# Kernel tuning notes

Measured on AMD Instinct MI355X. Metric: run time of the kernel, lower is better.

Reference implementation:

```python
import jax, jax.numpy as jnp
import numpy as np

B, T, S, D = 8, 16, 256, 1024
H, KVH, HD = 16, 4, 64
GROUPS = H // KVH
SCALE = HD ** -0.5
CAP = 50.0
EPS = 1e-6


def setup_inputs() -> dict:
    key = jax.random.key(0)
    ks = jax.random.split(key, 5)
    return {
        "x": jax.random.normal(ks[0], (B, T, S, D), dtype=jnp.float32),
        "Wq": jax.random.normal(ks[1], (D, H * HD), dtype=jnp.float32) * (D ** -0.5),
        "Wk": jax.random.normal(ks[2], (D, KVH * HD), dtype=jnp.float32) * (D ** -0.5),
        "Wv": jax.random.normal(ks[3], (D, KVH * HD), dtype=jnp.float32) * (D ** -0.5),
        "Wo": jax.random.normal(ks[4], (H * HD, D), dtype=jnp.float32) * ((H * HD) ** -0.5),
        "q_norm_w": jnp.ones((HD,), dtype=jnp.float32),
        "k_norm_w": jnp.ones((HD,), dtype=jnp.float32),
    }


def _rmsnorm(x, w):
    rms = jnp.sqrt(jnp.mean(x * x, axis=-1, keepdims=True) + EPS)
    return x / rms * w


def reference(x, Wq, Wk, Wv, Wo, q_norm_w, k_norm_w):
    b, t, s, d = x.shape
    xf = x.reshape(b * t, s, d)                    # (BT, S, D)
    q = (xf @ Wq).reshape(b * t, s, H, HD).transpose(0, 2, 1, 3)   # (BT, H, S, hd)
    k = (xf @ Wk).reshape(b * t, s, KVH, HD).transpose(0, 2, 1, 3)  # (BT, KVH, S, hd)
    v = (xf @ Wv).reshape(b * t, s, KVH, HD).transpose(0, 2, 1, 3)
    q = _rmsnorm(q, q_norm_w)
    k = _rmsnorm(k, k_norm_w)
    if GROUPS > 1:
        k = jnp.repeat(k, GROUPS, axis=1)          # (BT, H, S, hd)
        v = jnp.repeat(v, GROUPS, axis=1)
    logits = jnp.einsum("bhqd,bhkd->bhqk", q, k) * SCALE
    logits = CAP * jnp.tanh(logits / CAP)          # soft cap
    attn = jax.nn.softmax(logits, axis=-1)
    out = jnp.einsum("bhqk,bhkd->bhqd", attn, v)   # (BT, H, S, hd)
    out = out.transpose(0, 2, 1, 3).reshape(b * t, s, H * HD)
    out = out @ Wo
    return out.reshape(b, t, s, d)
```

## Files before the change

kernel.cpp:

```cpp
#include <hip/hip_runtime.h>
#include <cstdint>
#include <cstddef>

typedef __bf16 bf16x8 __attribute__((ext_vector_type(8)));
typedef float f32x4 __attribute__((ext_vector_type(4)));
typedef unsigned short u16;
typedef unsigned int u32;
typedef unsigned short u16x8 __attribute__((ext_vector_type(8)));

#define ROWS 32768
#define DMODEL 1024
#define NQKV 1536
#define C1_ 0.0072134752044448170f
#define A2_ 144.26950408889634f
#define B2_ 72.13475204444817f

__device__ __forceinline__ u16 f2bf(float f) {
    unsigned u = __float_as_uint(f);
    u += 0x7fffu + ((u >> 16) & 1u);
    return (u16)(u >> 16);
}
__device__ __forceinline__ float bf_lo(u32 u) { return __uint_as_float(u << 16); }
__device__ __forceinline__ float bf_hi(u32 u) { return __uint_as_float(u & 0xffff0000u); }
__device__ __forceinline__ u32 pack_rne(float lo, float hi) {
    return (u32)f2bf(lo) | ((u32)f2bf(hi) << 16);
}

__global__ __launch_bounds__(256) void f32_to_bf16_vec(
    const float* __restrict__ in, u16* __restrict__ out, int n4)
{
    int i = blockIdx.x * 256 + threadIdx.x;
    if (i >= n4) return;
    float4 f = ((const float4*)in)[i];
    ushort4 u;
    u.x = f2bf(f.x); u.y = f2bf(f.y); u.z = f2bf(f.z); u.w = f2bf(f.w);
    ((ushort4*)out)[i] = u;
}

__global__ __launch_bounds__(256) void transpose_bf16(
    const float* __restrict__ src, u16* __restrict__ dst, int R, int C)
{
    __shared__ float tile[32][33];
    int c0 = blockIdx.x * 32;
    int r0 = blockIdx.y * 32;
    int tx = threadIdx.x & 31;
    int ty = threadIdx.x >> 5;
#pragma unroll
    for (int i = 0; i < 32; i += 8)
        tile[ty + i][tx] = src[(size_t)(r0 + ty + i) * C + (c0 + tx)];
    __syncthreads();
#pragma unroll
    for (int i = 0; i < 32; i += 8)
        dst[(size_t)(c0 + ty + i) * R + (r0 + tx)] = f2bf(tile[tx][ty + i]);
}

template<bool BF16OUT>
__global__ __launch_bounds__(256) void gemm_bt(
    const u16* __restrict__ A, const u16* __restrict__ Bt,
    void* __restrict__ Cout, int M, int N, int K)
{
    __shared__ u16 As[128][32];
    __shared__ u16 Bs[128][32];
    const int tid  = threadIdx.x;
    const int wave = tid >> 6;
    const int lane = tid & 63;
    const int q4   = lane >> 4;
    const int cl   = lane & 15;
    const int wr   = wave >> 1, wc = wave & 1;
    const int m0   = blockIdx.x * 128;
    const int n0   = blockIdx.y * 128;
    const int srow = lane >> 2;
    const int skoff = (lane & 3) * 8;

    const f32x4 zero = {0.f, 0.f, 0.f, 0.f};
    f32x4 acc[4][4];
#pragma unroll
    for (int i = 0; i < 4; ++i)
#pragma unroll
        for (int j = 0; j < 4; ++j) acc[i][j] = zero;

    for (int k0 = 0; k0 < K; k0 += 32) {
        __syncthreads();
#pragma unroll
        for (int cc = 0; cc < 2; ++cc) {
            int r = 32 * wave + 16 * cc + srow;
            const u16* ga = A + (size_t)(m0 + r) * K + k0 + skoff;
            __builtin_amdgcn_global_load_lds(
                (const __attribute__((address_space(1))) void*)ga,
                (__attribute__((address_space(3))) void*)(&As[32 * wave + 16 * cc][0]),
                16, 0, 0);
            const u16* gb = Bt + (size_t)(n0 + r) * K + k0 + skoff;
            __builtin_amdgcn_global_load_lds(
                (const __attribute__((address_space(1))) void*)gb,
                (__attribute__((address_space(3))) void*)(&Bs[32 * wave + 16 * cc][0]),
                16, 0, 0);
        }
        __syncthreads();
        bf16x8 af[4], bfr[4];
#pragma unroll
        for (int i = 0; i < 4; ++i)
            af[i] = *(const bf16x8*)&As[64 * wr + 16 * i + cl][q4 * 8];
#pragma unroll
        for (int j = 0; j < 4; ++j)
            bfr[j] = *(const bf16x8*)&Bs[64 * wc + 16 * j + cl][q4 * 8];
#pragma unroll
        for (int i = 0; i < 4; ++i)
#pragma unroll
            for (int j = 0; j < 4; ++j)
                acc[i][j] = __builtin_amdgcn_mfma_f32_16x16x32_bf16(
                    af[i], bfr[j], acc[i][j], 0, 0, 0);
    }

#pragma unroll
    for (int i = 0; i < 4; ++i)
#pragma unroll
        for (int j = 0; j < 4; ++j)
#pragma unroll
            for (int r = 0; r < 4; ++r) {
                int row = m0 + 64 * wr + 16 * i + q4 * 4 + r;
                int col = n0 + 64 * wc + 16 * j + cl;
                if (BF16OUT)
                    ((u16*)Cout)[(size_t)row * N + col] = f2bf(acc[i][j][r]);
                else
                    ((float*)Cout)[(size_t)row * N + col] = acc[i][j][r];
            }
}

__global__ __launch_bounds__(256, 3) void attention_kernel(
    const u16* __restrict__ qkv, const float* __restrict__ qw,
    const float* __restrict__ kw, u16* __restrict__ ao)
{
    const int bi  = blockIdx.x;
    const int bt  = bi >> 4;
    const int h   = bi & 15;
    const int kvh = h >> 2;
    const int tid  = threadIdx.x;
    const int wave = tid >> 6;
    const int lane = tid & 63;
    const int q4   = lane >> 4;
    const int cl   = lane & 15;

    __shared__ __align__(16) u16 Vt[64][264];
    __shared__ __align__(16) u16 P[4][64][40];

    {
        const u16* vrow = qkv + (size_t)(bt * 256 + tid) * NQKV + 1280 + kvh * 64;
#pragma unroll
        for (int ch = 0; ch < 8; ++ch) {
            u16x8 v8 = *(const u16x8*)(vrow + ch * 8);
#pragma unroll
            for (int e = 0; e < 8; ++e) Vt[ch * 8 + e][tid] = v8[e];
        }
    }
    __syncthreads();

    const u16* qbase = qkv + (size_t)(bt * 256) * NQKV + h * 64;
    const u16* kbase = qkv + (size_t)(bt * 256) * NQKV + 1024 + kvh * 64;

    uint4 qa[2][4];
    float rq[4];
    float wqk[2][8];
#pragma unroll
    for (int ks = 0; ks < 2; ++ks)
#pragma unroll
        for (int e = 0; e < 8; ++e) {
            int d = ks * 32 + q4 * 8 + e;
            wqk[ks][e] = qw[d] * kw[d];
        }
#pragma unroll
    for (int i = 0; i < 4; ++i) {
#pragma unroll
        for (int ks = 0; ks < 2; ++ks)
            qa[ks][i] = *(const uint4*)(qbase +
                (size_t)(wave * 64 + 16 * i + cl) * NQKV + ks * 32 + q4 * 8);
        float ss = 0.f;
#pragma unroll
        for (int ks = 0; ks < 2; ++ks) {
            const u32* u = (const u32*)&qa[ks][i];
#pragma unroll
            for (int e = 0; e < 4; ++e) {
                float lo = bf_lo(u[e]), hi = bf_hi(u[e]);
                ss += lo * lo + hi * hi;
            }
        }
        ss += __shfl_xor(ss, 16, 64);
        ss += __shfl_xor(ss, 32, 64);
        rq[i] = rsqrtf(ss * (1.0f / 64.0f) + 1e-6f);
#pragma unroll
        for (int ks = 0; ks < 2; ++ks) {
            u32* u = (u32*)&qa[ks][i];
#pragma unroll
            for (int e = 0; e < 4; ++e) {
                float lo = bf_lo(u[e]) * wqk[ks][2 * e];
                float hi = bf_hi(u[e]) * wqk[ks][2 * e + 1];
                u[e] = pack_rne(lo, hi);
            }
        }
    }
    float rqc[4][4];
#pragma unroll
    for (int i = 0; i < 4; ++i)
#pragma unroll
        for (int r = 0; r < 4; ++r)
            rqc[i][r] = __shfl(rq[i], 4 * q4 + r, 64);

    const f32x4 zero = {0.f, 0.f, 0.f, 0.f};
    f32x4 o[4][4];
    f32x4 lacc[4];
#pragma unroll
    for (int i = 0; i < 4; ++i) {
        lacc[i] = zero;
#pragma unroll
        for (int j = 0; j < 4; ++j) o[i][j] = zero;
    }
    bf16x8 ones;
#pragma unroll
    for (int e = 0; e < 8; ++e) ones[e] = (__bf16)1.0f;

    for (int nb = 0; nb < 4; ++nb) {
#pragma unroll
        for (int jh = 0; jh < 2; ++jh) {
#pragma unroll
            for (int jj = 0; jj < 2; ++jj) {
                const int j = 2 * jh + jj;
                uint4 kb[2];
#pragma unroll
                for (int ks = 0; ks < 2; ++ks)
                    kb[ks] = *(const uint4*)(kbase +
                        (size_t)(nb * 64 + 16 * j + cl) * NQKV + ks * 32 + q4 * 8);
                float ss = 0.f;
#pragma unroll
                for (int ks = 0; ks < 2; ++ks) {
                    const u32* u = (const u32*)&kb[ks];
#pragma unroll
                    for (int e = 0; e < 4; ++e) {
                        float lo = bf_lo(u[e]), hi = bf_hi(u[e]);
                        ss += lo * lo + hi * hi;
                    }
                }
                ss += __shfl_xor(ss, 16, 64);
                ss += __shfl_xor(ss, 32, 64);
                float rkc1 = rsqrtf(ss * (1.0f / 64.0f) + 1e-6f) * C1_;

#pragma unroll
                for (int i = 0; i < 4; ++i) {
                    f32x4 s = __builtin_amdgcn_mfma_f32_16x16x32_bf16(
                        *(const bf16x8*)&qa[0][i], *(const bf16x8*)&kb[0], zero, 0, 0, 0);
                    s = __builtin_amdgcn_mfma_f32_16x16x32_bf16(
                        *(const bf16x8*)&qa[1][i], *(const bf16x8*)&kb[1], s, 0, 0, 0);
#pragma unroll
                    for (int r = 0; r < 4; ++r) {
                        float e2 = __builtin_amdgcn_exp2f(s[r] * rqc[i][r] * rkc1);
                        float rc = __builtin_amdgcn_rcpf(e2 + 1.0f);
                        float p  = __builtin_amdgcn_exp2f(fmaf(-A2_, rc, B2_));
                        P[wave][16 * i + q4 * 4 + r][16 * jj + cl] = f2bf(p);
                    }
                }
            }
            bf16x8 vb[4];
#pragma unroll
            for (int j2 = 0; j2 < 4; ++j2)
                vb[j2] = *(const bf16x8*)&Vt[16 * j2 + cl][nb * 64 + jh * 32 + q4 * 8];
#pragma unroll
            for (int i = 0; i < 4; ++i) {
                bf16x8 pa = *(const bf16x8*)&P[wave][16 * i + cl][q4 * 8];
#pragma unroll
                for (int j2 = 0; j2 < 4; ++j2)
                    o[i][j2] = __builtin_amdgcn_mfma_f32_16x16x32_bf16(
                        pa, vb[j2], o[i][j2], 0, 0, 0);
                lacc[i] = __builtin_amdgcn_mfma_f32_16x16x32_bf16(
                    pa, ones, lacc[i], 0, 0, 0);
            }
        }
    }

#pragma unroll
    for (int i = 0; i < 4; ++i)
#pragma unroll
        for (int r = 0; r < 4; ++r) {
            float inv = 1.0f / lacc[i][r];
            int row = bt * 256 + wave * 64 + 16 * i + q4 * 4 + r;
#pragma unroll
            for (int j = 0; j < 4; ++j) {
                int col = h * 64 + 16 * j + cl;
                ao[(size_t)row * DMODEL + col] = f2bf(o[i][j][r] * inv);
            }
        }
}

extern "C" void kernel_launch(void* const* d_in, const int* in_sizes, int n_in,
                              void* d_out, int out_size, void* d_ws, size_t ws_size,
                              hipStream_t stream)
{
    const float* x  = (const float*)d_in[0];
    const float* Wq = (const float*)d_in[1];
    const float* Wk = (const float*)d_in[2];
    const float* Wv = (const float*)d_in[3];
    const float* Wo = (const float*)d_in[4];
    const float* qw = (const float*)d_in[5];
    const float* kw = (const float*)d_in[6];
    float* out = (float*)d_out;

    char* ws = (char*)d_ws;
    u16* Xb  = (u16*)(ws);
    u16* QKV = (u16*)(ws + (size_t)67108864);
    u16* AO  = (u16*)(ws + (size_t)167772160);
    u16* WcT = (u16*)(ws + (size_t)234881024);
    u16* WoT = (u16*)(ws + (size_t)238026752);

    f32_to_bf16_vec<<<dim3(32768), dim3(256), 0, stream>>>(x, Xb, 8388608);
    transpose_bf16<<<dim3(32, 32), dim3(256), 0, stream>>>(Wq, WcT, 1024, 1024);
    transpose_bf16<<<dim3(8, 32), dim3(256), 0, stream>>>(Wk, WcT + (size_t)1024 * 1024, 1024, 256);
    transpose_bf16<<<dim3(8, 32), dim3(256), 0, stream>>>(Wv, WcT + (size_t)1280 * 1024, 1024, 256);
    transpose_bf16<<<dim3(32, 32), dim3(256), 0, stream>>>(Wo, WoT, 1024, 1024);
    gemm_bt<true><<<dim3(256, 12), dim3(256), 0, stream>>>(Xb, WcT, (void*)QKV, ROWS, NQKV, 1024);
    attention_kernel<<<dim3(2048), dim3(256), 0, stream>>>(QKV, qw, kw, AO);
    gemm_bt<false><<<dim3(256, 8), dim3(256), 0, stream>>>(AO, WoT, (void*)out, ROWS, DMODEL, 1024);
}
```

Measured before the change: 660.1 us.

## Keep attention probabilities in registers via transposed S=K·Q MFMA layout

The QK^T product is computed transposed (K as the A operand, Q as B), so each lane's accumulator output already matches the B-operand layout of a 16x16x16 bf16 MFMA. The probabilities can then be packed in registers and fed straight into the PV and row-sum MFMAs, which removes the per-wave shared-memory P buffer and its store/load round trip. Output is written as vectorized 8-byte packed stores, and the K-norm shuffle moves into the inner loop. The tradeoff is smaller K=16 MFMAs (twice as many instructions for PV), more shuffles per K tile, and a fully unrolled nb loop that may raise register pressure.

Measured after the change: 674.3 us. 1.02x slower.

```diff
diff --git a/kernel.cpp b/kernel.cpp
--- a/kernel.cpp
+++ b/kernel.cpp
@@ -1,9 +1,11 @@
 #include <hip/hip_runtime.h>
+#include <hip/hip_bf16.h>
 #include <cstdint>
 #include <cstddef>
 
 typedef __bf16 bf16x8 __attribute__((ext_vector_type(8)));
 typedef float f32x4 __attribute__((ext_vector_type(4)));
+typedef short s16x4 __attribute__((ext_vector_type(4)));
 typedef unsigned short u16;
 typedef unsigned int u32;
 typedef unsigned short u16x8 __attribute__((ext_vector_type(8)));
@@ -24,6 +26,11 @@
 __device__ __forceinline__ float bf_hi(u32 u) { return __uint_as_float(u & 0xffff0000u); }
 __device__ __forceinline__ u32 pack_rne(float lo, float hi) {
     return (u32)f2bf(lo) | ((u32)f2bf(hi) << 16);
+}
+__device__ __forceinline__ u32 pk2(float lo, float hi) {
+    union { __hip_bfloat162 b; u32 u; } c;
+    c.b = __float22bfloat162_rn(float2{lo, hi});
+    return c.u;
 }
 
 __global__ __launch_bounds__(256) void f32_to_bf16_vec(
@@ -141,7 +148,6 @@
     const int cl   = lane & 15;
 
     __shared__ __align__(16) u16 Vt[64][264];
-    __shared__ __align__(16) u16 P[4][64][40];
 
     {
         const u16* vrow = qkv + (size_t)(bt * 256 + tid) * NQKV + 1280 + kvh * 64;
@@ -168,15 +174,15 @@
             wqk[ks][e] = qw[d] * kw[d];
         }
 #pragma unroll
-    for (int i = 0; i < 4; ++i) {
+    for (int qi = 0; qi < 4; ++qi) {
 #pragma unroll
         for (int ks = 0; ks < 2; ++ks)
-            qa[ks][i] = *(const uint4*)(qbase +
-                (size_t)(wave * 64 + 16 * i + cl) * NQKV + ks * 32 + q4 * 8);
+            qa[ks][qi] = *(const uint4*)(qbase +
+                (size_t)(wave * 64 + 16 * qi + cl) * NQKV + ks * 32 + q4 * 8);
         float ss = 0.f;
 #pragma unroll
         for (int ks = 0; ks < 2; ++ks) {
-            const u32* u = (const u32*)&qa[ks][i];
+            const u32* u = (const u32*)&qa[ks][qi];
 #pragma unroll
             for (int e = 0; e < 4; ++e) {
                 float lo = bf_lo(u[e]), hi = bf_hi(u[e]);
@@ -185,10 +191,10 @@
         }
         ss += __shfl_xor(ss, 16, 64);
         ss += __shfl_xor(ss, 32, 64);
-        rq[i] = rsqrtf(ss * (1.0f / 64.0f) + 1e-6f);
+        rq[qi] = rsqrtf(ss * (1.0f / 64.0f) + 1e-6f);
 #pragma unroll
         for (int ks = 0; ks < 2; ++ks) {
-            u32* u = (u32*)&qa[ks][i];
+            u32* u = (u32*)&qa[ks][qi];
 #pragma unroll
             for (int e = 0; e < 4; ++e) {
                 float lo = bf_lo(u[e]) * wqk[ks][2 * e];
@@ -197,95 +203,101 @@
             }
         }
     }
-    float rqc[4][4];
-#pragma unroll
-    for (int i = 0; i < 4; ++i)
-#pragma unroll
-        for (int r = 0; r < 4; ++r)
-            rqc[i][r] = __shfl(rq[i], 4 * q4 + r, 64);
 
     const f32x4 zero = {0.f, 0.f, 0.f, 0.f};
     f32x4 o[4][4];
     f32x4 lacc[4];
 #pragma unroll
-    for (int i = 0; i < 4; ++i) {
-        lacc[i] = zero;
-#pragma unroll
-        for (int j = 0; j < 4; ++j) o[i][j] = zero;
-    }
-    bf16x8 ones;
-#pragma unroll
-    for (int e = 0; e < 8; ++e) ones[e] = (__bf16)1.0f;
-
+    for (int dj = 0; dj < 4; ++dj) {
+        lacc[dj] = zero;
+#pragma unroll
+        for (int qi = 0; qi < 4; ++qi) o[dj][qi] = zero;
+    }
+    s16x4 ones16;
+#pragma unroll
+    for (int e = 0; e < 4; ++e) ones16[e] = (short)0x3F80;
+
+#pragma unroll
     for (int nb = 0; nb < 4; ++nb) {
 #pragma unroll
-        for (int jh = 0; jh < 2; ++jh) {
-#pragma unroll
-            for (int jj = 0; jj < 2; ++jj) {
-                const int j = 2 * jh + jj;
-                uint4 kb[2];
-#pragma unroll
-                for (int ks = 0; ks < 2; ++ks)
-                    kb[ks] = *(const uint4*)(kbase +
-                        (size_t)(nb * 64 + 16 * j + cl) * NQKV + ks * 32 + q4 * 8);
-                float ss = 0.f;
-#pragma unroll
-                for (int ks = 0; ks < 2; ++ks) {
-                    const u32* u = (const u32*)&kb[ks];
-#pragma unroll
-                    for (int e = 0; e < 4; ++e) {
-                        float lo = bf_lo(u[e]), hi = bf_hi(u[e]);
-                        ss += lo * lo + hi * hi;
-                    }
+        for (int si = 0; si < 4; ++si) {
+            uint4 kb0 = *(const uint4*)(kbase +
+                (size_t)(nb * 64 + 16 * si + cl) * NQKV + q4 * 8);
+            uint4 kb1 = *(const uint4*)(kbase +
+                (size_t)(nb * 64 + 16 * si + cl) * NQKV + 32 + q4 * 8);
+            float ss = 0.f;
+            {
+                const u32* u0 = (const u32*)&kb0;
+                const u32* u1 = (const u32*)&kb1;
+#pragma unroll
+                for (int e = 0; e < 4; ++e) {
+                    float a = bf_lo(u0[e]), b = bf_hi(u0[e]);
+                    float c = bf_lo(u1[e]), d = bf_hi(u1[e]);
+                    ss += a * a + b * b + c * c + d * d;
                 }
-                ss += __shfl_xor(ss, 16, 64);
-                ss += __shfl_xor(ss, 32, 64);
-                float rkc1 = rsqrtf(ss * (1.0f / 64.0f) + 1e-6f) * C1_;
-
-#pragma unroll
-                for (int i = 0; i < 4; ++i) {
-                    f32x4 s = __builtin_amdgcn_mfma_f32_16x16x32_bf16(
-                        *(const bf16x8*)&qa[0][i], *(const bf16x8*)&kb[0], zero, 0, 0, 0);
-                    s = __builtin_amdgcn_mfma_f32_16x16x32_bf16(
-                        *(const bf16x8*)&qa[1][i], *(const bf16x8*)&kb[1], s, 0, 0, 0);
-#pragma unroll
-                    for (int r = 0; r < 4; ++r) {
-                        float e2 = __builtin_amdgcn_exp2f(s[r] * rqc[i][r] * rkc1);
-                        float rc = __builtin_amdgcn_rcpf(e2 + 1.0f);
-                        float p  = __builtin_amdgcn_exp2f(fmaf(-A2_, rc, B2_));
-                        P[wave][16 * i + q4 * 4 + r][16 * jj + cl] = f2bf(p);
-                    }
+            }
+            ss += __shfl_xor(ss, 16, 64);
+            ss += __shfl_xor(ss, 32, 64);
+            float rk = rsqrtf(ss * (1.0f / 64.0f) + 1e-6f);
+            float cr[4];
+#pragma unroll
+            for (int r = 0; r < 4; ++r)
+                cr[r] = __shfl(rk, 4 * q4 + r, 64) * C1_;
+
+            f32x4 st[4];
+#pragma unroll
+            for (int qi = 0; qi < 4; ++qi) {
+                st[qi] = __builtin_amdgcn_mfma_f32_16x16x32_bf16(
+                    *(const bf16x8*)&kb0, *(const bf16x8*)&qa[0][qi], zero, 0, 0, 0);
+                st[qi] = __builtin_amdgcn_mfma_f32_16x16x32_bf16(
+                    *(const bf16x8*)&kb1, *(const bf16x8*)&qa[1][qi], st[qi], 0, 0, 0);
+            }
+
+            s16x4 pf[4];
+#pragma unroll
+            for (int qi = 0; qi < 4; ++qi) {
+                float p[4];
+#pragma unroll
+                for (int r = 0; r < 4; ++r) {
+                    float e2 = __builtin_amdgcn_exp2f(st[qi][r] * rq[qi] * cr[r]);
+                    float rc = __builtin_amdgcn_rcpf(e2 + 1.0f);
+                    p[r] = __builtin_amdgcn_exp2f(fmaf(-A2_, rc, B2_));
                 }
-            }
-            bf16x8 vb[4];
-#pragma unroll
-            for (int j2 = 0; j2 < 4; ++j2)
-                vb[j2] = *(const bf16x8*)&Vt[16 * j2 + cl][nb * 64 + jh * 32 + q4 * 8];
-#pragma unroll
-            for (int i = 0; i < 4; ++i) {
-                bf16x8 pa = *(const bf16x8*)&P[wave][16 * i + cl][q4 * 8];
-#pragma unroll
-                for (int j2 = 0; j2 < 4; ++j2)
-                    o[i][j2] = __builtin_amdgcn_mfma_f32_16x16x32_bf16(
-                        pa, vb[j2], o[i][j2], 0, 0, 0);
-                lacc[i] = __builtin_amdgcn_mfma_f32_16x16x32_bf16(
-                    pa, ones, lacc[i], 0, 0, 0);
-            }
-        }
-    }
-
-#pragma unroll
-    for (int i = 0; i < 4; ++i)
-#pragma unroll
-        for (int r = 0; r < 4; ++r) {
-            float inv = 1.0f / lacc[i][r];
-            int row = bt * 256 + wave * 64 + 16 * i + q4 * 4 + r;
-#pragma unroll
-            for (int j = 0; j < 4; ++j) {
-                int col = h * 64 + 16 * j + cl;
-                ao[(size_t)row * DMODEL + col] = f2bf(o[i][j][r] * inv);
-            }
-        }
+                union { u32 u[2]; s16x4 s; } pkd;
+                pkd.u[0] = pk2(p[0], p[1]);
+                pkd.u[1] = pk2(p[2], p[3]);
+                pf[qi] = pkd.s;
+            }
+
+#pragma unroll
+            for (int qi = 0; qi < 4; ++qi)
+                lacc[qi] = __builtin_amdgcn_mfma_f32_16x16x16bf16_1k(
+                    ones16, pf[qi], lacc[qi], 0, 0, 0);
+
+#pragma unroll
+            for (int dj = 0; dj < 4; ++dj) {
+                s16x4 vf = *(const s16x4*)&Vt[16 * dj + cl][nb * 64 + 16 * si + 4 * q4];
+#pragma unroll
+                for (int qi = 0; qi < 4; ++qi)
+                    o[dj][qi] = __builtin_amdgcn_mfma_f32_16x16x16bf16_1k(
+                        vf, pf[qi], o[dj][qi], 0, 0, 0);
+            }
+        }
+    }
+
+#pragma unroll
+    for (int qi = 0; qi < 4; ++qi) {
+        float inv = __builtin_amdgcn_rcpf(lacc[qi][0]);
+        int row = bt * 256 + wave * 64 + 16 * qi + cl;
+        u16* orow = ao + (size_t)row * DMODEL + h * 64 + 4 * q4;
+#pragma unroll
+        for (int dj = 0; dj < 4; ++dj) {
+            uint2 w;
+            w.x = pk2(o[dj][qi][0] * inv, o[dj][qi][1] * inv);
+            w.y = pk2(o[dj][qi][2] * inv, o[dj][qi][3] * inv);
+            *(uint2*)(orow + 16 * dj) = w;
+        }
+    }
 }
 
 extern "C" void kernel_launch(void* const* d_in, const int* in_sizes, int n_in,
```
